# Kernel tuning notes

Hardware: AMD Instinct MI355X
Metric: run time of the kernel (lower is better)

Reference implementation:

```python
import jax, jax.numpy as jnp
import numpy as np

N, E = 384, 3072          # nodes, relation pairs
CIN, EMB, D = 4096, 200, 512  # roi feat dim, glove dim, hidden dim
NOBJ, NREL = 151, 51
NUM_ITER = 3
ALPHA = 0.5


def setup_inputs() -> dict:
    key = jax.random.key(0)
    ks = iter(jax.random.split(key, 64))

    def w(shape, scale=0.02):
        return jax.random.normal(next(ks), shape, dtype=jnp.float32) * scale

    inp = {
        'x': jax.random.normal(next(ks), (N, CIN), dtype=jnp.float32),
        'pos_info': jax.random.uniform(next(ks), (N, 9), dtype=jnp.float32),
        'union_features': jax.random.normal(next(ks), (E, CIN), dtype=jnp.float32),
        'obj_labels': jax.random.randint(next(ks), (N,), 0, NOBJ, dtype=jnp.int32),
        'rel_pair_idx': jax.random.randint(next(ks), (E, 2), 0, N, dtype=jnp.int32),
        # embeddings
        'obj_embed1_w': w((NOBJ, EMB)),
        'obj_embed2_w': w((NOBJ, EMB)),
        # node/edge embeddings
        'node_emb_w': w((D, CIN + EMB + 128)), 'node_emb_b': jnp.zeros((D,)),
        'node_emb2_w': w((D, CIN + EMB + D)), 'node_emb2_b': jnp.zeros((D,)),
        'edge_emb_w': w((D, CIN)), 'edge_emb_b': jnp.zeros((D,)),
        # pos_embed: Linear(9,32) -> BN(32) -> Linear(32,128) -> ReLU
        'pos_w1': w((32, 9)), 'pos_b1': jnp.zeros((32,)),
        'pos_gamma': jnp.ones((32,)), 'pos_beta': jnp.zeros((32,)),
        'pos_w2': w((128, 32)), 'pos_b2': jnp.zeros((128,)),
        # node GRUCell (with bias), edge GRUCell (no bias); gate order r,z,n
        'ngate_wih': w((3 * D, D)), 'ngate_whh': w((3 * D, D)),
        'ngate_bih': jnp.zeros((3 * D,)), 'ngate_bhh': jnp.zeros((3 * D,)),
        'egate_wih': w((3 * D, D)), 'egate_whh': w((3 * D, D)),
        # message kernels
        'n2n_w1': w((D, D)), 'n2n_b1': jnp.zeros((D,)),
        'n2n_w2': w((D, D)), 'n2n_b2': jnp.zeros((D,)),
        'e2n_w1': w((D, D)), 'e2n_b1': jnp.zeros((D,)),
        'e2n_w2': w((D, D)), 'e2n_b2': jnp.zeros((D,)),
        # node2edge 1x1 convs == pointwise linears
        'n2e_w1': w((D, 2 * D)), 'n2e_b1': jnp.zeros((D,)),
        'n2e_w2': w((D, D)), 'n2e_b2': jnp.zeros((D,)),
        'rel_cls_w': w((NREL, D)), 'rel_cls_b': jnp.zeros((NREL,)),
    }
    return inp


def _gru(x, h, wih, whh, bih=None, bhh=None):
    gi = x @ wih.T
    gh = h @ whh.T
    if bih is not None:
        gi = gi + bih
        gh = gh + bhh
    ir, iz, ig = jnp.split(gi, 3, axis=-1)
    hr, hz, hg = jnp.split(gh, 3, axis=-1)
    r = jax.nn.sigmoid(ir + hr)
    z = jax.nn.sigmoid(iz + hz)
    g = jnp.tanh(ig + r * hg)
    return (1.0 - z) * g + z * h


def _mlp2(h, w1, b1, w2, b2):
    h = jax.nn.relu(h @ w1.T + b1)
    return jax.nn.relu(h @ w2.T + b2)


def reference(x, pos_info, union_features, obj_labels, rel_pair_idx,
              obj_embed1_w, obj_embed2_w,
              node_emb_w, node_emb_b, node_emb2_w, node_emb2_b,
              edge_emb_w, edge_emb_b,
              pos_w1, pos_b1, pos_gamma, pos_beta, pos_w2, pos_b2,
              ngate_wih, ngate_whh, ngate_bih, ngate_bhh,
              egate_wih, egate_whh,
              n2n_w1, n2n_b1, n2n_w2, n2n_b2,
              e2n_w1, e2n_b1, e2n_w2, e2n_b2,
              n2e_w1, n2e_b1, n2e_w2, n2e_b2,
              rel_cls_w, rel_cls_b):
    n = x.shape[0]
    # pos embed (BatchNorm in training mode = batch stats)
    ph = pos_info @ pos_w1.T + pos_b1
    mu, var = ph.mean(0), ph.var(0)
    ph = (ph - mu) * jax.lax.rsqrt(var + 1e-5) * pos_gamma + pos_beta
    pos_embed = jax.nn.relu(ph @ pos_w2.T + pos_b2)

    obj_embed = obj_embed1_w[obj_labels]  # predcls: GT labels
    node_states = jnp.concatenate([x, obj_embed, pos_embed], -1) @ node_emb_w.T + node_emb_b

    p0, p1 = rel_pair_idx[:, 0], rel_pair_idx[:, 1]
    adj = jnp.zeros((n, n), jnp.float32).at[p0, p1].set(1.0)
    edge_rep = union_features @ edge_emb_w.T + edge_emb_b
    # torch sparse to_dense sums duplicate indices
    edge_states = jnp.zeros((n, n, D), jnp.float32).at[p0, p1].add(edge_rep)

    deg = adj.sum(1, keepdims=True) + 1e-6
    for _ in range(NUM_ITER):
        n2n = (adj @ node_states) / deg
        e2n = jnp.einsum('ij,ijd->jd', adj, edge_states)
        n2n = _mlp2(n2n, n2n_w1, n2n_b1, n2n_w2, n2n_b2)
        e2n = _mlp2(e2n, e2n_w1, e2n_b1, e2n_w2, e2n_b2)
        node_states = _gru(ALPHA * n2n + (1.0 - ALPHA) * e2n, node_states,
                           ngate_wih, ngate_whh, ngate_bih, ngate_bhh)

    # predcls: obj_dists = to_onehot(labels), preds = labels
    obj_dists = jnp.full((n, NOBJ), -1000.0, jnp.float32).at[jnp.arange(n), obj_labels].set(1000.0)
    node_states = jnp.concatenate([x, node_states, obj_embed2_w[obj_labels]], -1) @ node_emb2_w.T + node_emb2_b

    for _ in range(NUM_ITER):
        # all-pairs direction-aware concat, masked by adjacency
        ek = jnp.concatenate([
            jnp.broadcast_to(node_states[:, None, :], (n, n, D)),
            jnp.broadcast_to(node_states[None, :, :], (n, n, D)),
        ], -1) * adj[:, :, None]                      # [n, n, 2D]
        msg = _mlp2(ek, n2e_w1, n2e_b1, n2e_w2, n2e_b2)  # 1x1 convs == pointwise
        edge_states = _gru(msg.reshape(n * n, D), edge_states.reshape(n * n, D),
                           egate_wih, egate_whh).reshape(n, n, D)

    rel_feats = edge_states[p0, p1]
    rel_dists = rel_feats @ rel_cls_w.T + rel_cls_b
    return obj_dists, rel_dists
```

## Files before the change

kernel.cpp:

```cpp
#include <hip/hip_runtime.h>

typedef unsigned short ushort_t;
typedef unsigned int uint_t;

#define N_    384
#define E_    3072
#define CIN_  4096
#define EMB_  200
#define D_    512
#define NOBJ_ 151
#define NREL_ 51
#define K1_   (CIN_ + EMB_ + 128)
#define K1P_  4448
#define K2_   (CIN_ + EMB_ + D_)
#define K2P_  4832

__device__ __forceinline__ ushort_t f2b(float f) {
    uint_t u = __float_as_uint(f);
    u += 0x7FFFu + ((u >> 16) & 1u);
    return (ushort_t)(u >> 16);
}

__global__ void k_pair_min(const int* __restrict__ rp, int* __restrict__ mapMin) {
    int e = blockIdx.x * blockDim.x + threadIdx.x;
    if (e >= E_) return;
    atomicMin(&mapMin[rp[2 * e] * N_ + rp[2 * e + 1]], e);
}
__global__ void k_pair_rep(const int* __restrict__ rp, const int* __restrict__ mapMin,
                           int* __restrict__ rep, int* __restrict__ deg_cnt) {
    int e = blockIdx.x * blockDim.x + threadIdx.x;
    if (e >= E_) return;
    int r = mapMin[rp[2 * e] * N_ + rp[2 * e + 1]];
    rep[e] = r;
    if (r == e) atomicAdd(&deg_cnt[rp[2 * e]], 1);
}
__global__ void k_inv_deg(const int* __restrict__ deg_cnt, float* __restrict__ inv_deg) {
    int i = blockIdx.x * blockDim.x + threadIdx.x;
    if (i < N_) inv_deg[i] = 1.0f / ((float)deg_cnt[i] + 1e-6f);
}

__global__ __launch_bounds__(1024) void k_pos_a(const float* __restrict__ pi,
                                                const float* __restrict__ w1,
                                                const float* __restrict__ b1,
                                                const float* __restrict__ g,
                                                const float* __restrict__ be,
                                                float* __restrict__ posn) {
    __shared__ float ph[N_ * 32];
    __shared__ float mu_s[32], rs_s[32];
    int tid = threadIdx.x;
    for (int idx = tid; idx < N_ * 32; idx += 1024) {
        int i = idx >> 5, f = idx & 31;
        float s = b1[f];
        for (int k = 0; k < 9; ++k) s += pi[i * 9 + k] * w1[f * 9 + k];
        ph[idx] = s;
    }
    __syncthreads();
    if (tid < 32) {
        float s = 0.f;
        for (int i = 0; i < N_; ++i) s += ph[i * 32 + tid];
        float m = s / N_;
        float v = 0.f;
        for (int i = 0; i < N_; ++i) { float d = ph[i * 32 + tid] - m; v += d * d; }
        mu_s[tid] = m;
        rs_s[tid] = rsqrtf(v / N_ + 1e-5f);
    }
    __syncthreads();
    for (int idx = tid; idx < N_ * 32; idx += 1024) {
        int f = idx & 31;
        posn[idx] = (ph[idx] - mu_s[f]) * rs_s[f] * g[f] + be[f];
    }
}
__global__ void k_pos2(const float* __restrict__ pn, const float* __restrict__ w,
                       const float* __restrict__ b, float* __restrict__ out) {
    int idx = blockIdx.x * blockDim.x + threadIdx.x;
    if (idx >= N_ * 128) return;
    int i = idx / 128, f = idx % 128;
    float s = b[f];
    for (int k = 0; k < 32; ++k) s += pn[i * 32 + k] * w[f * 32 + k];
    out[idx] = fmaxf(s, 0.f);
}

__global__ void k_build_A1b(const float* __restrict__ x, const int* __restrict__ lab,
                            const float* __restrict__ emb1, const float* __restrict__ pe,
                            ushort_t* __restrict__ A) {
    int idx = blockIdx.x * blockDim.x + threadIdx.x;
    if (idx >= N_ * K1P_) return;
    int i = idx / K1P_, c = idx % K1P_;
    float v = 0.f;
    if (c < CIN_)             v = x[(size_t)i * CIN_ + c];
    else if (c < CIN_ + EMB_) v = emb1[lab[i] * EMB_ + (c - CIN_)];
    else if (c < K1_)         v = pe[i * 128 + (c - CIN_ - EMB_)];
    A[idx] = f2b(v);
}
__global__ void k_build_A2b(const float* __restrict__ x, const int* __restrict__ lab,
                            const float* __restrict__ emb2, const float* __restrict__ ns,
                            ushort_t* __restrict__ A) {
    int idx = blockIdx.x * blockDim.x + threadIdx.x;
    if (idx >= N_ * K2P_) return;
    int i = idx / K2P_, c = idx % K2P_;
    float v = 0.f;
    if (c < CIN_)             v = x[(size_t)i * CIN_ + c];
    else if (c < CIN_ + D_)   v = ns[i * D_ + (c - CIN_)];
    else if (c < K2_)         v = emb2[lab[i] * EMB_ + (c - CIN_ - D_)];
    A[idx] = f2b(v);
}
__global__ void k_build_ekb(const int* __restrict__ rp, const float* __restrict__ ns,
                            ushort_t* __restrict__ ek) {
    int idx = blockIdx.x * blockDim.x + threadIdx.x;
    if (idx >= E_ * 2 * D_) return;
    int e = idx / (2 * D_), c = idx % (2 * D_);
    float v = (c < D_) ? ns[rp[2 * e] * D_ + c] : ns[rp[2 * e + 1] * D_ + (c - D_)];
    ek[idx] = f2b(v);
}

struct ConvDesc { const float* src; ushort_t* dst; int K, Kp, rows, rowsp; };
struct ConvArgs { ConvDesc d[16]; };
__global__ void k_conv_batch(ConvArgs a) {
    ConvDesc c = a.d[blockIdx.y];
    for (int row = blockIdx.x; row < c.rowsp; row += gridDim.x) {
        const float* src = c.src + (size_t)row * c.K;
        ushort_t* dst = c.dst + (size_t)row * c.Kp;
        bool inrow = row < c.rows;
        for (int k = threadIdx.x * 4; k < c.Kp; k += blockDim.x * 4) {
            uint2 ov = {0u, 0u};
            if (inrow && k < c.K) {
                float4 v = *(const float4*)(src + k);
                ov.x = (uint_t)f2b(v.x) | ((uint_t)f2b(v.y) << 16);
                ov.y = (uint_t)f2b(v.z) | ((uint_t)f2b(v.w) << 16);
            }
            *(uint2*)(dst + k) = ov;
        }
    }
}
__global__ void k_f2b_n(const float* __restrict__ s, ushort_t* __restrict__ d, int n) {
    int i = blockIdx.x * blockDim.x + threadIdx.x;
    if (i < n) d[i] = f2b(s[i]);
}

__global__ void k_scatter_edge(const float* __restrict__ er, const int* __restrict__ rep,
                               float* __restrict__ es) {
    int e = blockIdx.x;
    int d = blockIdx.y * 256 + threadIdx.x;
    atomicAdd(&es[(size_t)rep[e] * D_ + d], er[(size_t)e * D_ + d]);
}
__global__ void k_broadcast_es(const int* __restrict__ rep, float* __restrict__ es,
                               ushort_t* __restrict__ esb) {
    int idx = blockIdx.x * blockDim.x + threadIdx.x;
    if (idx >= E_ * D_) return;
    int e = idx / D_, d = idx % D_;
    float v = es[(size_t)rep[e] * D_ + d];
    es[idx] = v;
    esb[idx] = f2b(v);
}
__global__ void k_scatter_e2n(const int* __restrict__ rp, const int* __restrict__ rep,
                              const float* __restrict__ es, float* __restrict__ e2n) {
    int e = blockIdx.x;
    if (rep[e] != e) return;
    int d = blockIdx.y * 256 + threadIdx.x;
    atomicAdd(&e2n[rp[2 * e + 1] * D_ + d], es[(size_t)e * D_ + d]);
}
__global__ void k_scatter_n2n(const int* __restrict__ rp, const int* __restrict__ rep,
                              const float* __restrict__ ns, float* __restrict__ n2n) {
    int e = blockIdx.x;
    if (rep[e] != e) return;
    int d = blockIdx.y * 256 + threadIdx.x;
    atomicAdd(&n2n[rp[2 * e] * D_ + d], ns[rp[2 * e + 1] * D_ + d]);
}
__global__ void k_scale_rows_b(const float* __restrict__ a, const float* __restrict__ inv_deg,
                               ushort_t* __restrict__ ob) {
    int idx = blockIdx.x * blockDim.x + threadIdx.x;
    if (idx >= N_ * D_) return;
    ob[idx] = f2b(a[idx] * inv_deg[idx / D_]);
}
__global__ void k_combine_b(const float* __restrict__ araw, const float* __restrict__ b2,
                            const float* __restrict__ e2nm, ushort_t* __restrict__ o) {
    int idx = blockIdx.x * blockDim.x + threadIdx.x;
    if (idx >= N_ * D_) return;
    float a = fmaxf(araw[idx] + b2[idx & (D_ - 1)], 0.f);
    o[idx] = f2b(0.5f * a + 0.5f * e2nm[idx]);
}
__global__ void k_epi(const float* __restrict__ raw, const float* __restrict__ bias,
                      float* __restrict__ fo, ushort_t* __restrict__ bo,
                      int total, int colmask, int relu) {
    int idx = blockIdx.x * blockDim.x + threadIdx.x;
    if (idx >= total) return;
    float v = raw[idx] + bias[idx & colmask];
    if (relu) v = fmaxf(v, 0.f);
    if (fo) fo[idx] = v;
    if (bo) bo[idx] = f2b(v);
}
__global__ void k_epi_rel(const float* __restrict__ raw, const float* __restrict__ relb,
                          float* __restrict__ out) {
    int idx = blockIdx.x * blockDim.x + threadIdx.x;
    if (idx >= E_ * NREL_) return;
    int row = idx / NREL_, col = idx % NREL_;
    out[idx] = raw[row * 64 + col] + relb[col];
}
__global__ void k_gru(const float* __restrict__ gi, const float* __restrict__ gh,
                      const float* __restrict__ bih, const float* __restrict__ bhh,
                      float* __restrict__ h, ushort_t* __restrict__ hb, int M) {
    int idx = blockIdx.x * blockDim.x + threadIdx.x;
    if (idx >= M * D_) return;
    int m = idx / D_, d = idx % D_;
    size_t b3 = (size_t)m * 3 * D_;
    float ir = gi[b3 + d], iz = gi[b3 + D_ + d], ig = gi[b3 + 2 * D_ + d];
    float hr = gh[b3 + d], hz = gh[b3 + D_ + d], hg = gh[b3 + 2 * D_ + d];
    if (bih) { ir += bih[d]; iz += bih[D_ + d]; ig += bih[2 * D_ + d]; }
    if (bhh) { hr += bhh[d]; hz += bhh[D_ + d]; hg += bhh[2 * D_ + d]; }
    float r = 1.f / (1.f + expf(-(ir + hr)));
    float z = 1.f / (1.f + expf(-(iz + hz)));
    float g = tanhf(ig + r * hg);
    size_t hi = (size_t)m * D_ + d;
    float nv = (1.f - z) * g + z * h[hi];
    h[hi] = nv;
    if (hb) hb[hi] = f2b(nv);
}
__global__ void k_obj_dists(const int* __restrict__ lab, float* __restrict__ out) {
    int idx = blockIdx.x * blockDim.x + threadIdx.x;
    if (idx >= N_ * NOBJ_) return;
    out[idx] = (idx % NOBJ_ == lab[idx / NOBJ_]) ? 1000.f : -1000.f;
}

typedef __attribute__((ext_vector_type(8))) short sh8;
typedef __attribute__((ext_vector_type(4))) float f32x4;

#define GLOAD_LDS16(gp, lp)                                                        \
    __builtin_amdgcn_global_load_lds((__attribute__((address_space(1))) void*)(gp),\
                                     (__attribute__((address_space(3))) void*)(lp),\
                                     16, 0, 0)

template <int FM, int FN>
__device__ __forceinline__ void gemm_kloop(ushort_t* As, ushort_t* Bs,
                                           const ushort_t* __restrict__ A,
                                           const ushort_t* __restrict__ B,
                                           f32x4 (&acc)[FM][FN],
                                           int K, int ks0, int ks1, int bm, int bn) {
    constexpr int BM = FM * 32, BN = FN * 32;
    constexpr int ATILES = (BM + 63) / 64, BTILES = (BN + 63) / 64;
    const int tid = threadIdx.x;
    const int lane = tid & 63, wid = tid >> 6;
    const int wr = wid >> 1, wc = wid & 1;
    const int ar = tid >> 2, ac = (tid & 3) * 8;
    const int l15 = lane & 15, lg = lane >> 4;
    for (int ks = ks0; ks < ks1; ++ks) {
        int k0 = ks * 32;
#pragma unroll
        for (int i = 0; i < ATILES; ++i) {
            int r = i * 64 + ar;
            if ((BM & 63) == 0 || r < BM)
                GLOAD_LDS16(A + (size_t)(bm + r) * K + k0 + ac, &As[r * 32 + ac]);
        }
#pragma unroll
        for (int i = 0; i < BTILES; ++i) {
            int r = i * 64 + ar;
            if ((BN & 63) == 0 || r < BN)
                GLOAD_LDS16(B + (size_t)(bn + r) * K + k0 + ac, &Bs[r * 32 + ac]);
        }
        __syncthreads();
        sh8 af[FM], bf[FN];
#pragma unroll
        for (int m = 0; m < FM; ++m)
            af[m] = *(const sh8*)&As[(wr * FM * 16 + m * 16 + l15) * 32 + lg * 8];
#pragma unroll
        for (int n = 0; n < FN; ++n)
            bf[n] = *(const sh8*)&Bs[(wc * FN * 16 + n * 16 + l15) * 32 + lg * 8];
#pragma unroll
        for (int m = 0; m < FM; ++m)
#pragma unroll
            for (int n = 0; n < FN; ++n)
                acc[m][n] = __builtin_amdgcn_mfma_f32_16x16x32_bf16(af[m], bf[n], acc[m][n], 0, 0, 0);
        __syncthreads();
    }
}

template <int FM, int FN>
__global__ __launch_bounds__(256) void gemm_mfma(const ushort_t* __restrict__ A,
                                                 const ushort_t* __restrict__ B,
                                                 const float* __restrict__ bias,
                                                 float* __restrict__ C,
                                                 ushort_t* __restrict__ Cb,
                                                 int M, int N, int K, int relu) {
    __shared__ ushort_t As[FM * 32 * 32];
    __shared__ ushort_t Bs[FN * 32 * 32];
    const int bm = blockIdx.y * FM * 32, bn = blockIdx.x * FN * 32;
    f32x4 acc[FM][FN];
#pragma unroll
    for (int m = 0; m < FM; ++m)
#pragma unroll
        for (int n = 0; n < FN; ++n) acc[m][n] = (f32x4){0.f, 0.f, 0.f, 0.f};
    gemm_kloop<FM, FN>(As, Bs, A, B, acc, K, 0, K / 32, bm, bn);
    const int lane = threadIdx.x & 63, wid = threadIdx.x >> 6;
    const int l15 = lane & 15, lg = lane >> 4;
    const int r0 = bm + (wid >> 1) * FM * 16, c0 = bn + (wid & 1) * FN * 16;
#pragma unroll
    for (int m = 0; m < FM; ++m)
#pragma unroll
        for (int n = 0; n < FN; ++n)
#pragma unroll
            for (int j = 0; j < 4; ++j) {
                int row = r0 + m * 16 + lg * 4 + j;
                int col = c0 + n * 16 + l15;
                if (row < M && col < N) {
                    float v = acc[m][n][j] + (bias ? bias[col] : 0.f);
                    if (relu) v = fmaxf(v, 0.f);
                    if (C)  C[(size_t)row * N + col] = v;
                    if (Cb) Cb[(size_t)row * N + col] = f2b(v);
                }
            }
}

template <int FM, int FN>
__global__ __launch_bounds__(256) void gemm_splitk(const ushort_t* __restrict__ A,
                                                   const ushort_t* __restrict__ B,
                                                   float* __restrict__ C,
                                                   int M, int N, int K, int S) {
    __shared__ ushort_t As[FM * 32 * 32];
    __shared__ ushort_t Bs[FN * 32 * 32];
    const int nsteps = K / 32;
    const int ss = (nsteps + S - 1) / S;
    const int ks0 = blockIdx.z * ss;
    const int ks1 = min(nsteps, ks0 + ss);
    if (ks0 >= ks1) return;
    const int bm = blockIdx.y * FM * 32, bn = blockIdx.x * FN * 32;
    f32x4 acc[FM][FN];
#pragma unroll
    for (int m = 0; m < FM; ++m)
#pragma unroll
        for (int n = 0; n < FN; ++n) acc[m][n] = (f32x4){0.f, 0.f, 0.f, 0.f};
    gemm_kloop<FM, FN>(As, Bs, A, B, acc, K, ks0, ks1, bm, bn);
    const int lane = threadIdx.x & 63, wid = threadIdx.x >> 6;
    const int l15 = lane & 15, lg = lane >> 4;
    const int r0 = bm + (wid >> 1) * FM * 16, c0 = bn + (wid & 1) * FN * 16;
#pragma unroll
    for (int m = 0; m < FM; ++m)
#pragma unroll
        for (int n = 0; n < FN; ++n)
#pragma unroll
            for (int j = 0; j < 4; ++j) {
                int row = r0 + m * 16 + lg * 4 + j;
                int col = c0 + n * 16 + l15;
                if (row < M && col < N)
                    atomicAdd(&C[(size_t)row * N + col], acc[m][n][j]);
            }
}

static inline dim3 mgrid(int M, int N, int FM, int FN) {
    return dim3((N + FN * 32 - 1) / (FN * 32), (M + FM * 32 - 1) / (FM * 32));
}
static inline dim3 sgrid(int M, int N, int FM, int FN, int S) {
    dim3 g = mgrid(M, N, FM, FN);
    return dim3(g.x, g.y, S);
}

extern "C" void kernel_launch(void* const* d_in, const int* in_sizes, int n_in,
                              void* d_out, int out_size, void* d_ws, size_t ws_size,
                              hipStream_t stream) {
    const float* x      = (const float*)d_in[0];
    const float* posi   = (const float*)d_in[1];
    const float* unionf = (const float*)d_in[2];
    const int*   lab    = (const int*)d_in[3];
    const int*   rp     = (const int*)d_in[4];
    const float* emb1   = (const float*)d_in[5];
    const float* emb2   = (const float*)d_in[6];
    const float* nw     = (const float*)d_in[7];
    const float* nb     = (const float*)d_in[8];
    const float* nw2    = (const float*)d_in[9];
    const float* nb2    = (const float*)d_in[10];
    const float* ew     = (const float*)d_in[11];
    const float* eb     = (const float*)d_in[12];
    const float* pw1    = (const float*)d_in[13];
    const float* pb1    = (const float*)d_in[14];
    const float* pg     = (const float*)d_in[15];
    const float* pbe    = (const float*)d_in[16];
    const float* pw2    = (const float*)d_in[17];
    const float* pb2    = (const float*)d_in[18];
    const float* ngwih  = (const float*)d_in[19];
    const float* ngwhh  = (const float*)d_in[20];
    const float* ngbih  = (const float*)d_in[21];
    const float* ngbhh  = (const float*)d_in[22];
    const float* egwih  = (const float*)d_in[23];
    const float* egwhh  = (const float*)d_in[24];
    const float* n2nw1  = (const float*)d_in[25];
    const float* n2nb1  = (const float*)d_in[26];
    const float* n2nw2  = (const float*)d_in[27];
    const float* n2nb2  = (const float*)d_in[28];
    const float* e2nw1  = (const float*)d_in[29];
    const float* e2nb1  = (const float*)d_in[30];
    const float* e2nw2  = (const float*)d_in[31];
    const float* e2nb2  = (const float*)d_in[32];
    const float* n2ew1  = (const float*)d_in[33];
    const float* n2eb1  = (const float*)d_in[34];
    const float* n2ew2  = (const float*)d_in[35];
    const float* n2eb2  = (const float*)d_in[36];
    const float* relw   = (const float*)d_in[37];
    const float* relb   = (const float*)d_in[38];

    size_t off = 0;
    auto alloc = [&](size_t bytes) {
        off = (off + 255) & ~(size_t)255;
        char* p = (char*)d_ws + off;
        off += bytes;
        return (void*)p;
    };
    int*      mapMin  = (int*)alloc((size_t)N_ * N_ * 4);
    int*      rep     = (int*)alloc(E_ * 4);
    int*      deg_cnt = (int*)alloc(N_ * 4);
    float*    inv_deg = (float*)alloc(N_ * 4);
    float*    posn    = (float*)alloc(N_ * 32 * 4);
    float*    pe      = (float*)alloc(N_ * 128 * 4);
    float*    ns      = (float*)alloc((size_t)N_ * D_ * 4);
    ushort_t* nsb     = (ushort_t*)alloc((size_t)N_ * D_ * 2);
    float*    nsraw   = (float*)alloc((size_t)N_ * D_ * 4);
    char*     scrR    = (char*)alloc((size_t)(2 * N_ * D_ + N_ * D_ + 2 * N_ * 3 * D_) * 4);
    float*    n2n     = (float*)scrR;
    float*    tmpraw  = (float*)(scrR + (size_t)N_ * D_ * 4);
    float*    n2nmraw = (float*)(scrR + (size_t)2 * N_ * D_ * 4);
    float*    gin     = (float*)(scrR + (size_t)3 * N_ * D_ * 4);
    float*    ghn     = (float*)(scrR + (size_t)(3 * N_ * D_ + N_ * 3 * D_) * 4);
    const size_t scrBytes = (size_t)(3 * N_ * D_ + 2 * N_ * 3 * D_) * 4;
    float*    e2nm    = (float*)alloc((size_t)N_ * D_ * 4);
    float*    relraw  = (float*)alloc((size_t)E_ * 64 * 4);
    char*     unionU  = (char*)alloc((size_t)E_ * 2 * D_ * 2);
    ushort_t* A1b = (ushort_t*)unionU;
    ushort_t* A2b = (ushort_t*)unionU;
    ushort_t* ekb = (ushort_t*)unionU;
    char*     ufbU = (char*)alloc((size_t)E_ * CIN_ * 2);
    ushort_t* ufb = (ushort_t*)ufbU;
    float*    gie = (float*)ufbU;
    char*     erepU = (char*)alloc((size_t)E_ * D_ * 4);
    float*    erep  = (float*)erepU;
    ushort_t* erepb = (ushort_t*)erepU;
    ushort_t* msgb  = (ushort_t*)(erepU + (size_t)E_ * D_ * 2);
    float*    es    = (float*)alloc((size_t)E_ * D_ * 4);
    ushort_t* esb   = (ushort_t*)alloc((size_t)E_ * D_ * 2);
    float*    e2n   = (float*)alloc((size_t)N_ * D_ * 4);
    ushort_t* e2nb  = (ushort_t*)alloc((size_t)N_ * D_ * 2);
    ushort_t* tmpb  = (ushort_t*)alloc((size_t)N_ * D_ * 2);
    ushort_t* n2nb  = (ushort_t*)alloc((size_t)N_ * D_ * 2);
    ushort_t* xinb  = (ushort_t*)alloc((size_t)N_ * D_ * 2);
    float*    ghe   = (float*)alloc((size_t)E_ * 3 * D_ * 4);
    ushort_t* nwb     = (ushort_t*)alloc((size_t)D_ * K1P_ * 2);
    ushort_t* nw2b    = (ushort_t*)alloc((size_t)D_ * K2P_ * 2);
    ushort_t* ewb     = (ushort_t*)alloc((size_t)D_ * CIN_ * 2);
    ushort_t* ngwihb  = (ushort_t*)alloc((size_t)3 * D_ * D_ * 2);
    ushort_t* ngwhhb  = (ushort_t*)alloc((size_t)3 * D_ * D_ * 2);
    ushort_t* egwihb  = (ushort_t*)alloc((size_t)3 * D_ * D_ * 2);
    ushort_t* egwhhb  = (ushort_t*)alloc((size_t)3 * D_ * D_ * 2);
    ushort_t* n2nw1b  = (ushort_t*)alloc((size_t)D_ * D_ * 2);
    ushort_t* n2nw2b  = (ushort_t*)alloc((size_t)D_ * D_ * 2);
    ushort_t* e2nw1b  = (ushort_t*)alloc((size_t)D_ * D_ * 2);
    ushort_t* e2nw2b  = (ushort_t*)alloc((size_t)D_ * D_ * 2);
    ushort_t* n2ew1b  = (ushort_t*)alloc((size_t)D_ * 2 * D_ * 2);
    ushort_t* n2ew2b  = (ushort_t*)alloc((size_t)D_ * D_ * 2);
    ushort_t* relwb   = (ushort_t*)alloc((size_t)64 * D_ * 2);
    if (off > ws_size) return;

    float* out_obj = (float*)d_out;
    float* out_rel = (float*)d_out + N_ * NOBJ_;

    ConvArgs ca;
    int ci = 0;
    auto addc = [&](const float* s, ushort_t* dptr, int K, int Kp, int rows, int rowsp) {
        ca.d[ci++] = ConvDesc{s, dptr, K, Kp, rows, rowsp};
    };
    addc(nw,    nwb,    K1_,      K1P_,     D_,       D_);
    addc(nw2,   nw2b,   K2_,      K2P_,     D_,       D_);
    addc(ew,    ewb,    CIN_,     CIN_,     D_,       D_);
    addc(ngwih, ngwihb, D_,       D_,       3 * D_,   3 * D_);
    addc(ngwhh, ngwhhb, D_,       D_,       3 * D_,   3 * D_);
    addc(egwih, egwihb, D_,       D_,       3 * D_,   3 * D_);
    addc(egwhh, egwhhb, D_,       D_,       3 * D_,   3 * D_);
    addc(n2nw1, n2nw1b, D_,       D_,       D_,       D_);
    addc(n2nw2, n2nw2b, D_,       D_,       D_,       D_);
    addc(e2nw1, e2nw1b, D_,       D_,       D_,       D_);
    addc(e2nw2, e2nw2b, D_,       D_,       D_,       D_);
    addc(n2ew1, n2ew1b, 2 * D_,   2 * D_,   D_,       D_);
    addc(n2ew2, n2ew2b, D_,       D_,       D_,       D_);
    addc(relw,  relwb,  D_,       D_,       NREL_,    64);
    addc(unionf, ufb,   CIN_,     CIN_,     E_,       E_);
    for (; ci < 16;) ca.d[ci++] = ConvDesc{nullptr, nullptr, 4, 4, 0, 0};
    k_conv_batch<<<dim3(512, 15), 256, 0, stream>>>(ca);

    (void)hipMemsetAsync(mapMin, 0x7F, (size_t)N_ * N_ * 4, stream);
    (void)hipMemsetAsync(deg_cnt, 0, N_ * 4, stream);
    k_pair_min<<<(E_ + 255) / 256, 256, 0, stream>>>(rp, mapMin);
    k_pair_rep<<<(E_ + 255) / 256, 256, 0, stream>>>(rp, mapMin, rep, deg_cnt);
    k_inv_deg<<<(N_ + 255) / 256, 256, 0, stream>>>(deg_cnt, inv_deg);

    k_pos_a<<<1, 1024, 0, stream>>>(posi, pw1, pb1, pg, pbe, posn);
    k_pos2<<<(N_ * 128 + 255) / 256, 256, 0, stream>>>(posn, pw2, pb2, pe);

    k_build_A1b<<<((size_t)N_ * K1P_ + 255) / 256, 256, 0, stream>>>(x, lab, emb1, pe, A1b);
    (void)hipMemsetAsync(nsraw, 0, (size_t)N_ * D_ * 4, stream);
    gemm_splitk<1, 1><<<sgrid(N_, D_, 1, 1, 8), 256, 0, stream>>>(A1b, nwb, nsraw, N_, D_, K1P_, 8);
    k_epi<<<(N_ * D_ + 255) / 256, 256, 0, stream>>>(nsraw, nb, ns, nsb, N_ * D_, D_ - 1, 0);

    (void)hipMemsetAsync(erep, 0, (size_t)E_ * D_ * 4, stream);
    gemm_splitk<2, 2><<<sgrid(E_, D_, 2, 2, 2), 256, 0, stream>>>(ufb, ewb, erep, E_, D_, CIN_, 2);
    k_epi<<<((size_t)E_ * D_ + 255) / 256, 256, 0, stream>>>(erep, eb, erep, nullptr, E_ * D_, D_ - 1, 0);
    (void)hipMemsetAsync(es, 0, (size_t)E_ * D_ * 4, stream);
    k_scatter_edge<<<dim3(E_, 2), 256, 0, stream>>>(erep, rep, es);
    k_broadcast_es<<<(E_ * D_ + 255) / 256, 256, 0, stream>>>(rep, es, esb);

    (void)hipMemsetAsync(e2n, 0, (size_t)N_ * D_ * 4, stream);
    k_scatter_e2n<<<dim3(E_, 2), 256, 0, stream>>>(rp, rep, es, e2n);
    k_f2b_n<<<(N_ * D_ + 255) / 256, 256, 0, stream>>>(e2n, e2nb, N_ * D_);
    (void)hipMemsetAsync(scrR, 0, scrBytes, stream);
    gemm_splitk<1, 1><<<sgrid(N_, D_, 1, 1, 8), 256, 0, stream>>>(e2nb, e2nw1b, tmpraw, N_, D_, D_, 8);
    k_epi<<<(N_ * D_ + 255) / 256, 256, 0, stream>>>(tmpraw, e2nb1, nullptr, tmpb, N_ * D_, D_ - 1, 1);
    gemm_splitk<1, 1><<<sgrid(N_, D_, 1, 1, 8), 256, 0, stream>>>(tmpb, e2nw2b, n2nmraw, N_, D_, D_, 8);
    k_epi<<<(N_ * D_ + 255) / 256, 256, 0, stream>>>(n2nmraw, e2nb2, e2nm, nullptr, N_ * D_, D_ - 1, 1);

    for (int it = 0; it < 3; ++it) {
        (void)hipMemsetAsync(scrR, 0, scrBytes, stream);
        k_scatter_n2n<<<dim3(E_, 2), 256, 0, stream>>>(rp, rep, ns, n2n);
        k_scale_rows_b<<<(N_ * D_ + 255) / 256, 256, 0, stream>>>(n2n, inv_deg, n2nb);
        gemm_splitk<1, 1><<<sgrid(N_, D_, 1, 1, 8), 256, 0, stream>>>(n2nb, n2nw1b, tmpraw, N_, D_, D_, 8);
        k_epi<<<(N_ * D_ + 255) / 256, 256, 0, stream>>>(tmpraw, n2nb1, nullptr, tmpb, N_ * D_, D_ - 1, 1);
        gemm_splitk<1, 1><<<sgrid(N_, D_, 1, 1, 8), 256, 0, stream>>>(tmpb, n2nw2b, n2nmraw, N_, D_, D_, 8);
        k_combine_b<<<(N_ * D_ + 255) / 256, 256, 0, stream>>>(n2nmraw, n2nb2, e2nm, xinb);
        gemm_splitk<1, 1><<<sgrid(N_, 3 * D_, 1, 1, 4), 256, 0, stream>>>(xinb, ngwihb, gin, N_, 3 * D_, D_, 4);
        gemm_splitk<1, 1><<<sgrid(N_, 3 * D_, 1, 1, 4), 256, 0, stream>>>(nsb, ngwhhb, ghn, N_, 3 * D_, D_, 4);
        k_gru<<<(N_ * D_ + 255) / 256, 256, 0, stream>>>(gin, ghn, ngbih, ngbhh, ns, nsb, N_);
    }

    k_obj_dists<<<(N_ * NOBJ_ + 255) / 256, 256, 0, stream>>>(lab, out_obj);

    k_build_A2b<<<((size_t)N_ * K2P_ + 255) / 256, 256, 0, stream>>>(x, lab, emb2, ns, A2b);
    (void)hipMemsetAsync(nsraw, 0, (size_t)N_ * D_ * 4, stream);
    gemm_splitk<1, 1><<<sgrid(N_, D_, 1, 1, 8), 256, 0, stream>>>(A2b, nw2b, nsraw, N_, D_, K2P_, 8);
    k_epi<<<(N_ * D_ + 255) / 256, 256, 0, stream>>>(nsraw, nb2, ns, nsb, N_ * D_, D_ - 1, 0);

    k_build_ekb<<<((size_t)E_ * 2 * D_ + 255) / 256, 256, 0, stream>>>(rp, ns, ekb);
    gemm_mfma<2, 2><<<mgrid(E_, D_, 2, 2), 256, 0, stream>>>(ekb, n2ew1b, n2eb1, nullptr, erepb, E_, D_, 2 * D_, 1);
    gemm_mfma<2, 2><<<mgrid(E_, D_, 2, 2), 256, 0, stream>>>(erepb, n2ew2b, n2eb2, nullptr, msgb, E_, D_, D_, 1);
    gemm_mfma<2, 4><<<mgrid(E_, 3 * D_, 2, 4), 256, 0, stream>>>(msgb, egwihb, nullptr, gie, nullptr, E_, 3 * D_, D_, 0);
    for (int it = 0; it < 3; ++it) {
        gemm_mfma<2, 4><<<mgrid(E_, 3 * D_, 2, 4), 256, 0, stream>>>(esb, egwhhb, nullptr, ghe, nullptr, E_, 3 * D_, D_, 0);
        k_gru<<<(E_ * D_ + 255) / 256, 256, 0, stream>>>(gie, ghe, nullptr, nullptr, es, esb, E_);
    }

    (void)hipMemsetAsync(relraw, 0, (size_t)E_ * 64 * 4, stream);
    gemm_splitk<1, 1><<<sgrid(E_, 64, 1, 1, 4), 256, 0, stream>>>(esb, relwb, relraw, E_, 64, D_, 4);
    k_epi_rel<<<(E_ * NREL_ + 255) / 256, 256, 0, stream>>>(relraw, relb, out_rel);
}
```

Baseline: 705.0 us.

## Fuse edge GRU hidden GEMM with gate update and swizzle GEMM block order

```diff
diff --git a/kernel.cpp b/kernel.cpp
--- a/kernel.cpp
+++ b/kernel.cpp
@@ -93,24 +93,23 @@
     A[idx] = f2b(v);
 }
 __global__ void k_build_A2b(const float* __restrict__ x, const int* __restrict__ lab,
-                            const float* __restrict__ emb2, const float* __restrict__ ns,
+                            const float* __restrict__ emb2, const ushort_t* __restrict__ nsb,
                             ushort_t* __restrict__ A) {
     int idx = blockIdx.x * blockDim.x + threadIdx.x;
     if (idx >= N_ * K2P_) return;
     int i = idx / K2P_, c = idx % K2P_;
-    float v = 0.f;
-    if (c < CIN_)             v = x[(size_t)i * CIN_ + c];
-    else if (c < CIN_ + D_)   v = ns[i * D_ + (c - CIN_)];
-    else if (c < K2_)         v = emb2[lab[i] * EMB_ + (c - CIN_ - D_)];
-    A[idx] = f2b(v);
-}
-__global__ void k_build_ekb(const int* __restrict__ rp, const float* __restrict__ ns,
+    ushort_t o = 0;
+    if (c < CIN_)             o = f2b(x[(size_t)i * CIN_ + c]);
+    else if (c < CIN_ + D_)   o = nsb[i * D_ + (c - CIN_)];
+    else if (c < K2_)         o = f2b(emb2[lab[i] * EMB_ + (c - CIN_ - D_)]);
+    A[idx] = o;
+}
+__global__ void k_build_ekb(const int* __restrict__ rp, const ushort_t* __restrict__ nsb,
                             ushort_t* __restrict__ ek) {
     int idx = blockIdx.x * blockDim.x + threadIdx.x;
     if (idx >= E_ * 2 * D_) return;
     int e = idx / (2 * D_), c = idx % (2 * D_);
-    float v = (c < D_) ? ns[rp[2 * e] * D_ + c] : ns[rp[2 * e + 1] * D_ + (c - D_)];
-    ek[idx] = f2b(v);
+    ek[idx] = (c < D_) ? nsb[rp[2 * e] * D_ + c] : nsb[rp[2 * e + 1] * D_ + (c - D_)];
 }
 
 struct ConvDesc { const float* src; ushort_t* dst; int K, Kp, rows, rowsp; };
@@ -229,6 +228,20 @@
                                      (__attribute__((address_space(3))) void*)(lp),\
                                      16, 0, 0)
 
+template <bool SWZ>
+__device__ __forceinline__ void get_bxyz(int& bx, int& by, int& bz) {
+    if (!SWZ) { bx = blockIdx.x; by = blockIdx.y; bz = blockIdx.z; return; }
+    int nx = gridDim.x, nz = gridDim.z;
+    int bid = blockIdx.x + nx * (blockIdx.y + gridDim.y * blockIdx.z);
+    int r8 = bid & 7, i = bid >> 3;
+    int per = nx * nz;
+    int ygrp = i / per;
+    int rem = i - ygrp * per;
+    bx = rem % nx;
+    bz = rem / nx;
+    by = r8 + 8 * ygrp;
+}
+
 template <int FM, int FN>
 __device__ __forceinline__ void gemm_kloop(ushort_t* As, ushort_t* Bs,
                                            const ushort_t* __restrict__ A,
@@ -273,7 +286,7 @@
     }
 }
 
-template <int FM, int FN>
+template <int FM, int FN, bool SWZ = false>
 __global__ __launch_bounds__(256) void gemm_mfma(const ushort_t* __restrict__ A,
                                                  const ushort_t* __restrict__ B,
                                                  const float* __restrict__ bias,
@@ -282,7 +295,9 @@
                                                  int M, int N, int K, int relu) {
     __shared__ ushort_t As[FM * 32 * 32];
     __shared__ ushort_t Bs[FN * 32 * 32];
-    const int bm = blockIdx.y * FM * 32, bn = blockIdx.x * FN * 32;
+    int bx, by, bz;
+    get_bxyz<SWZ>(bx, by, bz);
+    const int bm = by * FM * 32, bn = bx * FN * 32;
     f32x4 acc[FM][FN];
 #pragma unroll
     for (int m = 0; m < FM; ++m)
@@ -309,19 +324,21 @@
             }
 }
 
-template <int FM, int FN>
+template <int FM, int FN, bool SWZ = false>
 __global__ __launch_bounds__(256) void gemm_splitk(const ushort_t* __restrict__ A,
                                                    const ushort_t* __restrict__ B,
                                                    float* __restrict__ C,
                                                    int M, int N, int K, int S) {
     __shared__ ushort_t As[FM * 32 * 32];
     __shared__ ushort_t Bs[FN * 32 * 32];
+    int bx, by, bz;
+    get_bxyz<SWZ>(bx, by, bz);
     const int nsteps = K / 32;
     const int ss = (nsteps + S - 1) / S;
-    const int ks0 = blockIdx.z * ss;
+    const int ks0 = bz * ss;
     const int ks1 = min(nsteps, ks0 + ss);
     if (ks0 >= ks1) return;
-    const int bm = blockIdx.y * FM * 32, bn = blockIdx.x * FN * 32;
+    const int bm = by * FM * 32, bn = bx * FN * 32;
     f32x4 acc[FM][FN];
 #pragma unroll
     for (int m = 0; m < FM; ++m)
@@ -342,6 +359,78 @@
                 if (row < M && col < N)
                     atomicAdd(&C[(size_t)row * N + col], acc[m][n][j]);
             }
+}
+
+__global__ __launch_bounds__(256) void k_ghe_gru(const ushort_t* __restrict__ esb_in,
+                                                 const ushort_t* __restrict__ W,
+                                                 const float* __restrict__ gi,
+                                                 const float* __restrict__ es_in,
+                                                 float* __restrict__ es_out,
+                                                 ushort_t* __restrict__ esb_out) {
+    __shared__ ushort_t As[64 * 32];
+    __shared__ ushort_t Bs[96 * 32];
+    int bid = blockIdx.x + gridDim.x * blockIdx.y;
+    int r8 = bid & 7, i = bid >> 3;
+    int per = gridDim.x;
+    int ygrp = i / per;
+    int x = i - ygrp * per;
+    int y = r8 + 8 * ygrp;
+    const int bm = y * 64;
+    const int dcol0 = x * 32;
+    const int tid = threadIdx.x;
+    const int lane = tid & 63, wid = tid >> 6;
+    const int wr = wid >> 1, wc = wid & 1;
+    const int ar = tid >> 2, ac = (tid & 3) * 8;
+    const int l15 = lane & 15, lg = lane >> 4;
+    f32x4 acc[2][3];
+#pragma unroll
+    for (int m = 0; m < 2; ++m)
+#pragma unroll
+        for (int g = 0; g < 3; ++g) acc[m][g] = (f32x4){0.f, 0.f, 0.f, 0.f};
+
+    for (int k0 = 0; k0 < D_; k0 += 32) {
+        GLOAD_LDS16(esb_in + (size_t)(bm + ar) * D_ + k0 + ac, &As[ar * 32 + ac]);
+        {
+            int rr = ar;
+            int wrow = (rr >> 5) * D_ + dcol0 + (rr & 31);
+            GLOAD_LDS16(W + (size_t)wrow * D_ + k0 + ac, &Bs[rr * 32 + ac]);
+        }
+        if (tid < 128) {
+            int rr = 64 + ar;
+            int wrow = 2 * D_ + dcol0 + (rr & 31);
+            GLOAD_LDS16(W + (size_t)wrow * D_ + k0 + ac, &Bs[rr * 32 + ac]);
+        }
+        __syncthreads();
+        sh8 af[2], bf[3];
+#pragma unroll
+        for (int m = 0; m < 2; ++m)
+            af[m] = *(const sh8*)&As[(wr * 32 + m * 16 + l15) * 32 + lg * 8];
+#pragma unroll
+        for (int g = 0; g < 3; ++g)
+            bf[g] = *(const sh8*)&Bs[(g * 32 + wc * 16 + l15) * 32 + lg * 8];
+#pragma unroll
+        for (int m = 0; m < 2; ++m)
+#pragma unroll
+            for (int g = 0; g < 3; ++g)
+                acc[m][g] = __builtin_amdgcn_mfma_f32_16x16x32_bf16(af[m], bf[g], acc[m][g], 0, 0, 0);
+        __syncthreads();
+    }
+
+    const int d = dcol0 + wc * 16 + l15;
+#pragma unroll
+    for (int m = 0; m < 2; ++m)
+#pragma unroll
+        for (int j = 0; j < 4; ++j) {
+            int row = bm + wr * 32 + m * 16 + lg * 4 + j;
+            size_t gbase = (size_t)row * 1536 + d;
+            float r = 1.f / (1.f + expf(-(gi[gbase] + acc[m][0][j])));
+            float z = 1.f / (1.f + expf(-(gi[gbase + 512] + acc[m][1][j])));
+            float g = tanhf(gi[gbase + 1024] + r * acc[m][2][j]);
+            float hv = es_in[(size_t)row * D_ + d];
+            float nv = (1.f - z) * g + z * hv;
+            es_out[(size_t)row * D_ + d] = nv;
+            esb_out[(size_t)row * D_ + d] = f2b(nv);
+        }
 }
 
 static inline dim3 mgrid(int M, int N, int FM, int FN) {
@@ -411,7 +500,7 @@
     float*    ns      = (float*)alloc((size_t)N_ * D_ * 4);
     ushort_t* nsb     = (ushort_t*)alloc((size_t)N_ * D_ * 2);
     float*    nsraw   = (float*)alloc((size_t)N_ * D_ * 4);
-    char*     scrR    = (char*)alloc((size_t)(2 * N_ * D_ + N_ * D_ + 2 * N_ * 3 * D_) * 4);
+    char*     scrR    = (char*)alloc((size_t)(3 * N_ * D_ + 2 * N_ * 3 * D_) * 4);
     float*    n2n     = (float*)scrR;
     float*    tmpraw  = (float*)(scrR + (size_t)N_ * D_ * 4);
     float*    n2nmraw = (float*)(scrR + (size_t)2 * N_ * D_ * 4);
@@ -433,12 +522,13 @@
     ushort_t* msgb  = (ushort_t*)(erepU + (size_t)E_ * D_ * 2);
     float*    es    = (float*)alloc((size_t)E_ * D_ * 4);
     ushort_t* esb   = (ushort_t*)alloc((size_t)E_ * D_ * 2);
+    float*    es2   = (float*)alloc((size_t)E_ * D_ * 4);
+    ushort_t* esb2  = (ushort_t*)alloc((size_t)E_ * D_ * 2);
     float*    e2n   = (float*)alloc((size_t)N_ * D_ * 4);
     ushort_t* e2nb  = (ushort_t*)alloc((size_t)N_ * D_ * 2);
     ushort_t* tmpb  = (ushort_t*)alloc((size_t)N_ * D_ * 2);
     ushort_t* n2nb  = (ushort_t*)alloc((size_t)N_ * D_ * 2);
     ushort_t* xinb  = (ushort_t*)alloc((size_t)N_ * D_ * 2);
-    float*    ghe   = (float*)alloc((size_t)E_ * 3 * D_ * 4);
     ushort_t* nwb     = (ushort_t*)alloc((size_t)D_ * K1P_ * 2);
     ushort_t* nw2b    = (ushort_t*)alloc((size_t)D_ * K2P_ * 2);
     ushort_t* ewb     = (ushort_t*)alloc((size_t)D_ * CIN_ * 2);
@@ -496,7 +586,7 @@
     k_epi<<<(N_ * D_ + 255) / 256, 256, 0, stream>>>(nsraw, nb, ns, nsb, N_ * D_, D_ - 1, 0);
 
     (void)hipMemsetAsync(erep, 0, (size_t)E_ * D_ * 4, stream);
-    gemm_splitk<2, 2><<<sgrid(E_, D_, 2, 2, 2), 256, 0, stream>>>(ufb, ewb, erep, E_, D_, CIN_, 2);
+    gemm_splitk<2, 2, true><<<sgrid(E_, D_, 2, 2, 4), 256, 0, stream>>>(ufb, ewb, erep, E_, D_, CIN_, 4);
     k_epi<<<((size_t)E_ * D_ + 255) / 256, 256, 0, stream>>>(erep, eb, erep, nullptr, E_ * D_, D_ - 1, 0);
     (void)hipMemsetAsync(es, 0, (size_t)E_ * D_ * 4, stream);
     k_scatter_edge<<<dim3(E_, 2), 256, 0, stream>>>(erep, rep, es);
@@ -526,21 +616,25 @@
 
     k_obj_dists<<<(N_ * NOBJ_ + 255) / 256, 256, 0, stream>>>(lab, out_obj);
 
-    k_build_A2b<<<((size_t)N_ * K2P_ + 255) / 256, 256, 0, stream>>>(x, lab, emb2, ns, A2b);
+    k_build_A2b<<<((size_t)N_ * K2P_ + 255) / 256, 256, 0, stream>>>(x, lab, emb2, nsb, A2b);
     (void)hipMemsetAsync(nsraw, 0, (size_t)N_ * D_ * 4, stream);
     gemm_splitk<1, 1><<<sgrid(N_, D_, 1, 1, 8), 256, 0, stream>>>(A2b, nw2b, nsraw, N_, D_, K2P_, 8);
     k_epi<<<(N_ * D_ + 255) / 256, 256, 0, stream>>>(nsraw, nb2, ns, nsb, N_ * D_, D_ - 1, 0);
 
-    k_build_ekb<<<((size_t)E_ * 2 * D_ + 255) / 256, 256, 0, stream>>>(rp, ns, ekb);
-    gemm_mfma<2, 2><<<mgrid(E_, D_, 2, 2), 256, 0, stream>>>(ekb, n2ew1b, n2eb1, nullptr, erepb, E_, D_, 2 * D_, 1);
-    gemm_mfma<2, 2><<<mgrid(E_, D_, 2, 2), 256, 0, stream>>>(erepb, n2ew2b, n2eb2, nullptr, msgb, E_, D_, D_, 1);
-    gemm_mfma<2, 4><<<mgrid(E_, 3 * D_, 2, 4), 256, 0, stream>>>(msgb, egwihb, nullptr, gie, nullptr, E_, 3 * D_, D_, 0);
-    for (int it = 0; it < 3; ++it) {
-        gemm_mfma<2, 4><<<mgrid(E_, 3 * D_, 2, 4), 256, 0, stream>>>(esb, egwhhb, nullptr, ghe, nullptr, E_, 3 * D_, D_, 0);
-        k_gru<<<(E_ * D_ + 255) / 256, 256, 0, stream>>>(gie, ghe, nullptr, nullptr, es, esb, E_);
-    }
-
-    (void)hipMemsetAsync(relraw, 0, (size_t)E_ * 64 * 4, stream);
-    gemm_splitk<1, 1><<<sgrid(E_, 64, 1, 1, 4), 256, 0, stream>>>(esb, relwb, relraw, E_, 64, D_, 4);
-    k_epi_rel<<<(E_ * NREL_ + 255) / 256, 256, 0, stream>>>(relraw, relb, out_rel);
-}
+    k_build_ekb<<<((size_t)E_ * 2 * D_ + 255) / 256, 256, 0, stream>>>(rp, nsb, ekb);
+    gemm_mfma<2, 2, true><<<mgrid(E_, D_, 2, 2), 256, 0, stream>>>(ekb, n2ew1b, n2eb1, nullptr, erepb, E_, D_, 2 * D_, 1);
+    gemm_mfma<2, 2, true><<<mgrid(E_, D_, 2, 2), 256, 0, stream>>>(erepb, n2ew2b, n2eb2, nullptr, msgb, E_, D_, D_, 1);
+    gemm_mfma<2, 4, true><<<mgrid(E_, 3 * D_, 2, 4), 256, 0, stream>>>(msgb, egwihb, nullptr, gie, nullptr, E_, 3 * D_, D_, 0);
+    {
+        float* esI = es;  ushort_t* esbI = esb;
+        float* esO = es2; ushort_t* esbO = esb2;
+        for (int it = 0; it < 3; ++it) {
+            k_ghe_gru<<<dim3(16, 48), 256, 0, stream>>>(esbI, egwhhb, gie, esI, esO, esbO);
+            float* tf = esI; esI = esO; esO = tf;
+            ushort_t* tb = esbI; esbI = esbO; esbO = tb;
+        }
+        (void)hipMemsetAsync(relraw, 0, (size_t)E_ * 64 * 4, stream);
+        gemm_splitk<1, 1><<<sgrid(E_, 64, 1, 1, 4), 256, 0, stream>>>(esbI, relwb, relraw, E_, 64, D_, 4);
+        k_epi_rel<<<(E_ * NREL_ + 255) / 256, 256, 0, stream>>>(relraw, relb, out_rel);
+    }
+}
```

Result: faster. 664.4 us (-5.8%).
